# Performance work log

Hardware: AMD Instinct MI355X
Metric: run time of the kernel (lower is better)

Reference implementation:

```python
import jax, jax.numpy as jnp
import numpy as np

B, DIN, H1, H2 = 16384, 512, 256, 128
S, DC, DE, T, TE, GH = 4, 4, 2, 3, 2, 64
NDOM = DC * DE            # 8 domain experts total
ETOT = S + NDOM + TE      # 14 experts feeding each task gate


def setup_inputs() -> dict:
    key = jax.random.key(0)
    ks = jax.random.split(key, 20)
    w = lambda k, shape, fan: (jax.random.normal(k, shape, jnp.float32) / np.sqrt(fan).astype(np.float32))
    x = jax.random.normal(ks[0], (B, DIN), jnp.float32)
    domain_ids = jax.random.randint(ks[1], (B,), 0, DC, jnp.int64) if jax.config.jax_enable_x64 else jax.random.randint(ks[1], (B,), 0, DC, jnp.int32)
    return {
        "x": x,
        "domain_ids": domain_ids,
        # shared experts (stacked): input->256->128, ReLU on both layers
        "sW1": w(ks[2], (S, DIN, H1), DIN), "sb1": jnp.zeros((S, H1), jnp.float32),
        "sW2": w(ks[3], (S, H1, H2), H1),   "sb2": jnp.zeros((S, H2), jnp.float32),
        # domain experts, all domains stacked in order domain0..domainDC-1
        "dW1": w(ks[4], (NDOM, DIN, H1), DIN), "db1": jnp.zeros((NDOM, H1), jnp.float32),
        "dW2": w(ks[5], (NDOM, H1, H2), H1),   "db2": jnp.zeros((NDOM, H2), jnp.float32),
        # task experts, all tasks stacked task0..taskT-1
        "tW1": w(ks[6], (T * TE, DIN, H1), DIN), "tb1": jnp.zeros((T * TE, H1), jnp.float32),
        "tW2": w(ks[7], (T * TE, H1, H2), H1),   "tb2": jnp.zeros((T * TE, H2), jnp.float32),
        # task gates (stacked over tasks): input->64 (ReLU) -> ETOT (linear) -> softmax
        "gW1": w(ks[8], (T, DIN, GH), DIN), "gb1": jnp.zeros((T, GH), jnp.float32),
        "gW2": w(ks[9], (T, GH, ETOT), GH), "gb2": jnp.zeros((T, ETOT), jnp.float32),
    }


def _experts(x, W1, b1, W2, b2):
    # x: [B, DIN]; W1: [E, DIN, H1]; W2: [E, H1, H2] -> [B, E, H2]
    h = jax.nn.relu(jnp.einsum('bi,eih->beh', x, W1) + b1)
    return jax.nn.relu(jnp.einsum('beh,eho->beo', h, W2) + b2)


def reference(x, domain_ids, sW1, sb1, sW2, sb2, dW1, db1, dW2, db2,
              tW1, tb1, tW2, tb2, gW1, gb1, gW2, gb2):
    shared = _experts(x, sW1, sb1, sW2, sb2)          # [B, S, H2]
    domain = _experts(x, dW1, db1, dW2, db2)          # [B, NDOM, H2]
    task = _experts(x, tW1, tb1, tW2, tb2)            # [B, T*TE, H2]
    task = task.reshape(B, T, TE, H2)
    base = jnp.concatenate([shared, domain], axis=1)  # [B, S+NDOM, H2]
    base = jnp.broadcast_to(base[:, None], (B, T, S + NDOM, H2))
    all_experts = jnp.concatenate([base, task], axis=2)  # [B, T, ETOT, H2]
    # task gates
    gh = jax.nn.relu(jnp.einsum('bi,tig->btg', x, gW1) + gb1)
    gates = jax.nn.softmax(jnp.einsum('btg,tge->bte', gh, gW2) + gb2, axis=-1)  # [B, T, ETOT]
    out = jnp.einsum('bteh,bte->tbh', all_experts, gates)  # [T, B, H2]
    # note: the torch per-sample domain_weighted_output is computed then discarded;
    # only these task outputs are returned, and they do not depend on domain_ids.
    return tuple(out[t] for t in range(T))
```

## Files before the change

### kernel.cpp

```cpp
#include <hip/hip_runtime.h>
#include <hip/hip_bf16.h>

#define NB 16384
#define DIN 512
#define H1 256
#define H2 128
#define NE 18
#define NT 3
#define NGH 64
#define NETOT 14

typedef float f32x4 __attribute__((ext_vector_type(4)));
typedef short s16x8 __attribute__((ext_vector_type(8)));
typedef short s16x4 __attribute__((ext_vector_type(4)));
typedef unsigned short u16;
typedef unsigned int u32;

__device__ __forceinline__ u16 f2bf(float f) {
    union { float f; u32 u; } v; v.f = f;
    u32 r = v.u + 0x7fffu + ((v.u >> 16) & 1u);
    return (u16)(r >> 16);
}
__device__ __forceinline__ float bf2f(u16 u) {
    union { u32 u; float f; } v; v.u = ((u32)u) << 16;
    return v.f;
}
__device__ __forceinline__ u32 cvtpk(float a, float b) {
    u32 r;
    asm("v_cvt_pk_bf16_f32 %0, %1, %2" : "=v"(r) : "v"(a), "v"(b));
    return r;
}

#define GLDS16(g, l) __builtin_amdgcn_global_load_lds((const u32*)(g), (u32*)(l), 16, 0, 0)
#define VMCNT0_BARRIER() do { asm volatile("s_waitcnt vmcnt(0)" ::: "memory"); __builtin_amdgcn_s_barrier(); } while (0)

__global__ __launch_bounds__(256) void k_prep(
    const float* __restrict__ x, u16* __restrict__ xb,
    const float* __restrict__ sW1, const float* __restrict__ dW1, const float* __restrict__ tW1,
    const float* __restrict__ sW2, const float* __restrict__ dW2, const float* __restrict__ tW2,
    const float* __restrict__ gW1, u16* __restrict__ w1t, u16* __restrict__ w2t, u16* __restrict__ gw1t)
{
    __shared__ float lds[64 * 65];
    int bx = blockIdx.x;
    if (bx < 8192) {
        int i = (bx * 256 + threadIdx.x) * 4;
        float4 v = *reinterpret_cast<const float4*>(x + i);
        ushort4 o;
        o.x = f2bf(v.x); o.y = f2bf(v.y); o.z = f2bf(v.z); o.w = f2bf(v.w);
        *reinterpret_cast<ushort4*>(xb + i) = o;
        return;
    }
    int b = bx - 8192;
    const float* src; u16* dst; int K, N, k0, n0;
    if (b < 576) {
        int e = b >> 5, tile = b & 31;
        src = (e < 4) ? sW1 + (size_t)e * DIN * H1 : (e < 12) ? dW1 + (size_t)(e - 4) * DIN * H1
                                                              : tW1 + (size_t)(e - 12) * DIN * H1;
        dst = w1t + (size_t)e * H1 * DIN; K = DIN; N = H1;
        k0 = (tile >> 2) * 64; n0 = (tile & 3) * 64;
    } else if (b < 720) {
        int b2 = b - 576; int e = b2 >> 3, tile = b2 & 7;
        src = (e < 4) ? sW2 + (size_t)e * H1 * H2 : (e < 12) ? dW2 + (size_t)(e - 4) * H1 * H2
                                                             : tW2 + (size_t)(e - 12) * H1 * H2;
        dst = w2t + (size_t)e * H2 * H1; K = H1; N = H2;
        k0 = (tile >> 1) * 64; n0 = (tile & 1) * 64;
    } else {
        int b3 = b - 720; int t = b3 >> 3, tile = b3 & 7;
        src = gW1 + (size_t)t * DIN * NGH; dst = gw1t + (size_t)t * NGH * DIN; K = DIN; N = NGH;
        k0 = tile * 64; n0 = 0;
    }
    int t = threadIdx.x;
#pragma unroll
    for (int i = 0; i < 16; ++i) {
        int idx = i * 256 + t;
        int kk = idx >> 6, nn = idx & 63;
        lds[kk * 65 + nn] = src[(size_t)(k0 + kk) * N + n0 + nn];
    }
    __syncthreads();
#pragma unroll
    for (int i = 0; i < 16; ++i) {
        int idx = i * 256 + t;
        int nn = idx >> 6, kk = idx & 63;
        dst[(size_t)(n0 + nn) * K + k0 + kk] = f2bf(lds[kk * 65 + nn]);
    }
}

__global__ __launch_bounds__(512, 4) void k_expert(
    const u16* __restrict__ xb, const u16* __restrict__ w1t, const u16* __restrict__ w2t,
    const float* __restrict__ sb1, const float* __restrict__ db1, const float* __restrict__ tb1,
    const float* __restrict__ sb2, const float* __restrict__ db2, const float* __restrict__ tb2,
    u16* __restrict__ eout)
{
    __shared__ __align__(128) char smem[65536];

    const int bx = blockIdx.x;
    const int e  = bx >> 7;
    const int m0 = (bx & 127) * 128;
    const int tid = threadIdx.x;
    const int w = tid >> 6, lane = tid & 63;
    const int wm = w & 1, wn = w >> 1;
    const int l15 = lane & 15, q = lane >> 4;
    const int q16 = q * 16;
    const int swk = ((l15 >> 1) & 3) << 4;
    const int swh = (l15 & 7) << 4;

    const u16* xg  = xb + (size_t)m0 * DIN;
    const u16* w1g = w1t + (size_t)e * H1 * DIN;
    const u16* w2g = w2t + (size_t)e * H2 * H1;
    const float* b1p = (e < 4) ? sb1 + e * H1 : (e < 12) ? db1 + (e - 4) * H1 : tb1 + (e - 12) * H1;
    const float* b2p = (e < 4) ? sb2 + e * H2 : (e < 12) ? db2 + (e - 4) * H2 : tb2 + (e - 12) * H2;

    const int sr = lane >> 2, sc = lane & 3;
    const int soff = (sc ^ ((lane >> 3) & 3)) * 8;
    const u16* gx   = xg  + (size_t)(w * 16 + sr) * DIN + soff;
    const u16* gw1a = w1g + (size_t)(w * 32 + sr) * DIN + soff;
    const u16* gw1b = w1g + (size_t)(w * 32 + 16 + sr) * DIN + soff;
    const int lx  = w * 1024;
    const int lwa = w * 2048;
    const int lwb = w * 2048 + 1024;

    int offX[4], offW[4];
#pragma unroll
    for (int mi = 0; mi < 4; ++mi)
        offX[mi] = (wm * 64 + mi * 16 + l15) * 64 + (q16 ^ swk);
#pragma unroll
    for (int nj = 0; nj < 4; ++nj)
        offW[nj] = (wn * 64 + nj * 16 + l15) * 64 + (q16 ^ swk);

    f32x4 acc1[4][4];
#pragma unroll
    for (int i = 0; i < 4; ++i)
#pragma unroll
        for (int j = 0; j < 4; ++j) acc1[i][j] = (f32x4)0.f;

    GLDS16(gx, smem + lx);
    GLDS16(gw1a, smem + 16384 + lwa);
    GLDS16(gw1b, smem + 16384 + lwb);
    VMCNT0_BARRIER();
    for (int kt = 0; kt < 16; ++kt) {
        if (kt < 15) {
            const int nb = (kt + 1) & 1, ko = (kt + 1) * 32;
            GLDS16(gx + ko, smem + nb * 8192 + lx);
            GLDS16(gw1a + ko, smem + 16384 + nb * 16384 + lwa);
            GLDS16(gw1b + ko, smem + 16384 + nb * 16384 + lwb);
        }
        const char* xbase = smem + (kt & 1) * 8192;
        const char* wbase = smem + 16384 + (kt & 1) * 16384;
        s16x8 xf[4], wf[4];
#pragma unroll
        for (int mi = 0; mi < 4; ++mi) xf[mi] = *(const s16x8*)(xbase + offX[mi]);
#pragma unroll
        for (int nj = 0; nj < 4; ++nj) wf[nj] = *(const s16x8*)(wbase + offW[nj]);
        __builtin_amdgcn_s_setprio(1);
#pragma unroll
        for (int mi = 0; mi < 4; ++mi)
#pragma unroll
            for (int nj = 0; nj < 4; ++nj)
                acc1[mi][nj] = __builtin_amdgcn_mfma_f32_16x16x32_bf16(wf[nj], xf[mi], acc1[mi][nj], 0, 0, 0);
        __builtin_amdgcn_s_setprio(0);
        VMCNT0_BARRIER();
    }

#pragma unroll
    for (int mi = 0; mi < 4; ++mi) {
        const int m = wm * 64 + mi * 16 + l15;
        char* rowp = smem + m * 512;
#pragma unroll
        for (int nj = 0; nj < 4; ++nj) {
            const float4 bv = *reinterpret_cast<const float4*>(b1p + wn * 64 + nj * 16 + q * 4);
            float v0 = fmaxf(acc1[mi][nj][0] + bv.x, 0.f);
            float v1 = fmaxf(acc1[mi][nj][1] + bv.y, 0.f);
            float v2 = fmaxf(acc1[mi][nj][2] + bv.z, 0.f);
            float v3 = fmaxf(acc1[mi][nj][3] + bv.w, 0.f);
            uint2 hv; hv.x = cvtpk(v0, v1); hv.y = cvtpk(v2, v3);
            const int b = wn * 128 + nj * 32 + q * 8;
            *reinterpret_cast<uint2*>(rowp + (b ^ swh)) = hv;
        }
    }
    __syncthreads();

    f32x4 acc2[4][2];
#pragma unroll
    for (int i = 0; i < 4; ++i)
#pragma unroll
        for (int j = 0; j < 2; ++j) acc2[i][j] = (f32x4)0.f;
    const u16* w2p0 = w2g + (size_t)(wn * 32 + l15) * H1 + q * 8;
    const u16* w2p1 = w2g + (size_t)(wn * 32 + 16 + l15) * H1 + q * 8;
#pragma unroll
    for (int kt2 = 0; kt2 < 8; ++kt2) {
        s16x8 wf2[2], hf[4];
        wf2[0] = *(const s16x8*)(w2p0 + kt2 * 32);
        wf2[1] = *(const s16x8*)(w2p1 + kt2 * 32);
#pragma unroll
        for (int mi = 0; mi < 4; ++mi) {
            const int m = wm * 64 + mi * 16 + l15;
            hf[mi] = *(const s16x8*)(smem + m * 512 + ((kt2 * 64 + q16) ^ swh));
        }
#pragma unroll
        for (int mi = 0; mi < 4; ++mi)
#pragma unroll
            for (int pj = 0; pj < 2; ++pj)
                acc2[mi][pj] = __builtin_amdgcn_mfma_f32_16x16x32_bf16(hf[mi], wf2[pj], acc2[mi][pj], 0, 0, 0);
    }

    u16* eo = eout + ((size_t)e * NB + m0) * H2;
#pragma unroll
    for (int mi = 0; mi < 4; ++mi)
#pragma unroll
        for (int pj = 0; pj < 2; ++pj) {
            const int p = wn * 32 + pj * 16 + l15;
            const float bias = b2p[p];
#pragma unroll
            for (int r = 0; r < 4; ++r) {
                const int row = wm * 64 + mi * 16 + q * 4 + r;
                float v = acc2[mi][pj][r] + bias;
                eo[(size_t)row * H2 + p] = f2bf(v > 0.f ? v : 0.f);
            }
        }
}

__global__ __launch_bounds__(256) void k_gate(
    const u16* __restrict__ xb, const u16* __restrict__ gw1t,
    const float* __restrict__ gb1, const float* __restrict__ gw2, const float* __restrict__ gb2,
    float* __restrict__ gates)
{
    __shared__ __align__(16) char smem[51200];
    u16* xs  = reinterpret_cast<u16*>(smem);
    u16* g1s = reinterpret_cast<u16*>(smem) + 4608;
    float* ghs = reinterpret_cast<float*>(smem);

    int m0 = blockIdx.x * 64;
    int tid = threadIdx.x;
    int w = tid >> 6, lane = tid & 63;
    int wm = w & 1, wn = w >> 1;
    int l15 = lane & 15, lk = (lane >> 4) * 8, lr4 = (lane >> 4) * 4;

    f32x4 acc[2][6];
#pragma unroll
    for (int i = 0; i < 2; ++i)
#pragma unroll
        for (int j = 0; j < 6; ++j) acc[i][j] = (f32x4)0.f;

    const u16* xg = xb + (size_t)m0 * DIN;
    int srow = tid >> 3, su = (tid & 7) * 8;
    for (int kc = 0; kc < DIN / 64; ++kc) {
#pragma unroll
        for (int it = 0; it < 2; ++it) {
            int rr = srow + it * 32;
            *reinterpret_cast<uint4*>(&xs[rr * 72 + su]) =
                *reinterpret_cast<const uint4*>(xg + (size_t)rr * DIN + kc * 64 + su);
        }
#pragma unroll
        for (int it = 0; it < 6; ++it) {
            int rr = srow + it * 32;
            *reinterpret_cast<uint4*>(&g1s[rr * 72 + su]) =
                *reinterpret_cast<const uint4*>(gw1t + (size_t)rr * DIN + kc * 64 + su);
        }
        __syncthreads();
        s16x8 af[2][2], bfr[6][2];
#pragma unroll
        for (int mi = 0; mi < 2; ++mi)
#pragma unroll
            for (int kk = 0; kk < 2; ++kk)
                af[mi][kk] = *reinterpret_cast<const s16x8*>(&xs[(wm * 32 + mi * 16 + l15) * 72 + kk * 32 + lk]);
#pragma unroll
        for (int nj = 0; nj < 6; ++nj)
#pragma unroll
            for (int kk = 0; kk < 2; ++kk)
                bfr[nj][kk] = *reinterpret_cast<const s16x8*>(&g1s[(wn * 96 + nj * 16 + l15) * 72 + kk * 32 + lk]);
#pragma unroll
        for (int kk = 0; kk < 2; ++kk)
#pragma unroll
            for (int mi = 0; mi < 2; ++mi)
#pragma unroll
                for (int nj = 0; nj < 6; ++nj)
                    acc[mi][nj] = __builtin_amdgcn_mfma_f32_16x16x32_bf16(af[mi][kk], bfr[nj][kk], acc[mi][nj], 0, 0, 0);
        __syncthreads();
    }
#pragma unroll
    for (int mi = 0; mi < 2; ++mi)
#pragma unroll
        for (int nj = 0; nj < 6; ++nj) {
            int col = wn * 96 + nj * 16 + l15;
            float bias = gb1[col];
#pragma unroll
            for (int r = 0; r < 4; ++r) {
                int row = wm * 32 + mi * 16 + lr4 + r;
                float v = acc[mi][nj][r] + bias;
                ghs[row * 200 + col] = v > 0.f ? v : 0.f;
            }
        }
    __syncthreads();

    if (tid < 192) {
        int tt = tid >> 6, rr = tid & 63;
        float logit[NETOT];
#pragma unroll
        for (int e2 = 0; e2 < NETOT; ++e2) logit[e2] = gb2[tt * NETOT + e2];
        const float* g2 = gw2 + tt * NGH * NETOT;
        const float* gr = &ghs[rr * 200 + tt * 64];
        for (int g = 0; g < NGH; ++g) {
            float v = gr[g];
#pragma unroll
            for (int e2 = 0; e2 < NETOT; ++e2) logit[e2] += v * g2[g * NETOT + e2];
        }
        float m = logit[0];
#pragma unroll
        for (int e2 = 1; e2 < NETOT; ++e2) m = fmaxf(m, logit[e2]);
        float s = 0.f, p[NETOT];
#pragma unroll
        for (int e2 = 0; e2 < NETOT; ++e2) { p[e2] = __expf(logit[e2] - m); s += p[e2]; }
        float inv = 1.f / s;
        float* go = gates + (size_t)(m0 + rr) * (NT * NETOT) + tt * NETOT;
#pragma unroll
        for (int e2 = 0; e2 < NETOT; ++e2) go[e2] = p[e2] * inv;
    }
}

__global__ __launch_bounds__(256) void k_combine(
    const u16* __restrict__ eout, const float* __restrict__ gates, float* __restrict__ out)
{
    int tid = threadIdx.x;
    int lr = tid >> 5, hq = tid & 31;
    int b = blockIdx.x * 8 + lr;
    int h0 = hq * 4;
    const float* g = gates + (size_t)b * (NT * NETOT);
    float o0[4] = {0, 0, 0, 0}, o1[4] = {0, 0, 0, 0}, o2[4] = {0, 0, 0, 0};
#pragma unroll
    for (int e = 0; e < NE; ++e) {
        ushort4 ev = *reinterpret_cast<const ushort4*>(&eout[((size_t)e * NB + b) * H2 + h0]);
        float v0 = bf2f(ev.x), v1 = bf2f(ev.y), v2 = bf2f(ev.z), v3 = bf2f(ev.w);
        if (e < 12) {
            float wa = g[e], wb = g[NETOT + e], wc = g[2 * NETOT + e];
            o0[0] += wa * v0; o0[1] += wa * v1; o0[2] += wa * v2; o0[3] += wa * v3;
            o1[0] += wb * v0; o1[1] += wb * v1; o1[2] += wb * v2; o1[3] += wb * v3;
            o2[0] += wc * v0; o2[1] += wc * v1; o2[2] += wc * v2; o2[3] += wc * v3;
        } else {
            int t = (e - 12) >> 1, te = (e - 12) & 1;
            float wt = g[t * NETOT + 12 + te];
            float* ot = (t == 0) ? o0 : (t == 1) ? o1 : o2;
            ot[0] += wt * v0; ot[1] += wt * v1; ot[2] += wt * v2; ot[3] += wt * v3;
        }
    }
    size_t base = (size_t)b * H2 + h0;
    *reinterpret_cast<float4*>(&out[0 * (size_t)NB * H2 + base]) = make_float4(o0[0], o0[1], o0[2], o0[3]);
    *reinterpret_cast<float4*>(&out[1 * (size_t)NB * H2 + base]) = make_float4(o1[0], o1[1], o1[2], o1[3]);
    *reinterpret_cast<float4*>(&out[2 * (size_t)NB * H2 + base]) = make_float4(o2[0], o2[1], o2[2], o2[3]);
}

extern "C" void kernel_launch(void* const* d_in, const int* in_sizes, int n_in,
                              void* d_out, int out_size, void* d_ws, size_t ws_size,
                              hipStream_t stream)
{
    const float* x   = (const float*)d_in[0];
    const float* sW1 = (const float*)d_in[2];
    const float* sb1 = (const float*)d_in[3];
    const float* sW2 = (const float*)d_in[4];
    const float* sb2 = (const float*)d_in[5];
    const float* dW1 = (const float*)d_in[6];
    const float* db1 = (const float*)d_in[7];
    const float* dW2 = (const float*)d_in[8];
    const float* db2 = (const float*)d_in[9];
    const float* tW1 = (const float*)d_in[10];
    const float* tb1 = (const float*)d_in[11];
    const float* tW2 = (const float*)d_in[12];
    const float* tb2 = (const float*)d_in[13];
    const float* gW1 = (const float*)d_in[14];
    const float* gb1 = (const float*)d_in[15];
    const float* gW2 = (const float*)d_in[16];
    const float* gb2 = (const float*)d_in[17];

    char* ws = (char*)d_ws;
    u16*  xb    = (u16*)(ws + 0);
    u16*  w1t   = (u16*)(ws + 16777216);
    u16*  w2t   = (u16*)(ws + 21495808);
    u16*  gw1t  = (u16*)(ws + 22675456);
    float* gates = (float*)(ws + 22872064);
    u16*  eout  = (u16*)(ws + 25624576);

    k_prep<<<dim3(8936), dim3(256), 0, stream>>>(x, xb, sW1, dW1, tW1, sW2, dW2, tW2, gW1, w1t, w2t, gw1t);
    k_gate<<<dim3(NB / 64), dim3(256), 0, stream>>>(xb, gw1t, gb1, gW2, gb2, gates);
    k_expert<<<dim3(NE * (NB / 128)), dim3(512), 0, stream>>>(xb, w1t, w2t, sb1, db1, tb1, sb2, db2, tb2, eout);
    k_combine<<<dim3(NB / 8), dim3(256), 0, stream>>>(eout, gates, (float*)d_out);
}
```

Baseline: 183.2 us.

## Fuse gate kernel into expert kernel and retile experts to 256-thread blocks

Merges the gate network into the expert kernel as extra trailing blocks, removing one launch and letting gate work overlap expert GEMMs. The expert kernel moves from 512 threads with a 2x4 wave grid to 256 threads where each wave owns all 128 rows and a 64-column slice. It also loosens the pipeline to wait with vmcnt(6) so the next tile's loads stay in flight during compute. The hidden buffer drops the XOR swizzle for padded 528-byte rows. In exchange, per-thread accumulators double, raising register pressure, and occupancy falls to two blocks per CU.

After: 148.1 us. 1.24x faster.

```diff
diff --git a/kernel.cpp b/kernel.cpp
--- a/kernel.cpp
+++ b/kernel.cpp
@@ -12,7 +12,6 @@
 
 typedef float f32x4 __attribute__((ext_vector_type(4)));
 typedef short s16x8 __attribute__((ext_vector_type(8)));
-typedef short s16x4 __attribute__((ext_vector_type(4)));
 typedef unsigned short u16;
 typedef unsigned int u32;
 
@@ -32,7 +31,6 @@
 }
 
 #define GLDS16(g, l) __builtin_amdgcn_global_load_lds((const u32*)(g), (u32*)(l), 16, 0, 0)
-#define VMCNT0_BARRIER() do { asm volatile("s_waitcnt vmcnt(0)" ::: "memory"); __builtin_amdgcn_s_barrier(); } while (0)
 
 __global__ __launch_bounds__(256) void k_prep(
     const float* __restrict__ x, u16* __restrict__ xb,
@@ -85,24 +83,118 @@
     }
 }
 
-__global__ __launch_bounds__(512, 4) void k_expert(
+__global__ __launch_bounds__(256, 2) void k_expert_gate(
     const u16* __restrict__ xb, const u16* __restrict__ w1t, const u16* __restrict__ w2t,
     const float* __restrict__ sb1, const float* __restrict__ db1, const float* __restrict__ tb1,
     const float* __restrict__ sb2, const float* __restrict__ db2, const float* __restrict__ tb2,
-    u16* __restrict__ eout)
+    u16* __restrict__ eout,
+    const u16* __restrict__ gw1t, const float* __restrict__ gb1,
+    const float* __restrict__ gw2, const float* __restrict__ gb2, float* __restrict__ gates)
 {
-    __shared__ __align__(128) char smem[65536];
-
-    const int bx = blockIdx.x;
-    const int e  = bx >> 7;
-    const int m0 = (bx & 127) * 128;
+    __shared__ __align__(128) char smem[67584];
+
+    const int bid = blockIdx.x;
     const int tid = threadIdx.x;
+
+    if (bid >= 2304) {
+        u16* xs  = reinterpret_cast<u16*>(smem);
+        u16* g1s = reinterpret_cast<u16*>(smem) + 4608;
+        float* ghs = reinterpret_cast<float*>(smem);
+
+        int m0 = (bid - 2304) * 64;
+        int w = tid >> 6, lane = tid & 63;
+        int wm = w & 1, wn = w >> 1;
+        int l15 = lane & 15, lk = (lane >> 4) * 8, lr4 = (lane >> 4) * 4;
+
+        f32x4 acc[2][6];
+#pragma unroll
+        for (int i = 0; i < 2; ++i)
+#pragma unroll
+            for (int j = 0; j < 6; ++j) acc[i][j] = (f32x4)0.f;
+
+        const u16* xg = xb + (size_t)m0 * DIN;
+        int srow = tid >> 3, su = (tid & 7) * 8;
+        for (int kc = 0; kc < DIN / 64; ++kc) {
+#pragma unroll
+            for (int it = 0; it < 2; ++it) {
+                int rr = srow + it * 32;
+                *reinterpret_cast<uint4*>(&xs[rr * 72 + su]) =
+                    *reinterpret_cast<const uint4*>(xg + (size_t)rr * DIN + kc * 64 + su);
+            }
+#pragma unroll
+            for (int it = 0; it < 6; ++it) {
+                int rr = srow + it * 32;
+                *reinterpret_cast<uint4*>(&g1s[rr * 72 + su]) =
+                    *reinterpret_cast<const uint4*>(gw1t + (size_t)rr * DIN + kc * 64 + su);
+            }
+            __syncthreads();
+            s16x8 af[2][2], bfr[6][2];
+#pragma unroll
+            for (int mi = 0; mi < 2; ++mi)
+#pragma unroll
+                for (int kk = 0; kk < 2; ++kk)
+                    af[mi][kk] = *reinterpret_cast<const s16x8*>(&xs[(wm * 32 + mi * 16 + l15) * 72 + kk * 32 + lk]);
+#pragma unroll
+            for (int nj = 0; nj < 6; ++nj)
+#pragma unroll
+                for (int kk = 0; kk < 2; ++kk)
+                    bfr[nj][kk] = *reinterpret_cast<const s16x8*>(&g1s[(wn * 96 + nj * 16 + l15) * 72 + kk * 32 + lk]);
+#pragma unroll
+            for (int kk = 0; kk < 2; ++kk)
+#pragma unroll
+                for (int mi = 0; mi < 2; ++mi)
+#pragma unroll
+                    for (int nj = 0; nj < 6; ++nj)
+                        acc[mi][nj] = __builtin_amdgcn_mfma_f32_16x16x32_bf16(af[mi][kk], bfr[nj][kk], acc[mi][nj], 0, 0, 0);
+            __syncthreads();
+        }
+#pragma unroll
+        for (int mi = 0; mi < 2; ++mi)
+#pragma unroll
+            for (int nj = 0; nj < 6; ++nj) {
+                int col = wn * 96 + nj * 16 + l15;
+                float bias = gb1[col];
+#pragma unroll
+                for (int r = 0; r < 4; ++r) {
+                    int row = wm * 32 + mi * 16 + lr4 + r;
+                    float v = acc[mi][nj][r] + bias;
+                    ghs[row * 200 + col] = v > 0.f ? v : 0.f;
+                }
+            }
+        __syncthreads();
+
+        if (tid < 192) {
+            int tt = tid >> 6, rr = tid & 63;
+            float logit[NETOT];
+#pragma unroll
+            for (int e2 = 0; e2 < NETOT; ++e2) logit[e2] = gb2[tt * NETOT + e2];
+            const float* g2 = gw2 + tt * NGH * NETOT;
+            const float* gr = &ghs[rr * 200 + tt * 64];
+            for (int g = 0; g < NGH; ++g) {
+                float v = gr[g];
+#pragma unroll
+                for (int e2 = 0; e2 < NETOT; ++e2) logit[e2] += v * g2[g * NETOT + e2];
+            }
+            float m = logit[0];
+#pragma unroll
+            for (int e2 = 1; e2 < NETOT; ++e2) m = fmaxf(m, logit[e2]);
+            float s = 0.f, p[NETOT];
+#pragma unroll
+            for (int e2 = 0; e2 < NETOT; ++e2) { p[e2] = __expf(logit[e2] - m); s += p[e2]; }
+            float inv = 1.f / s;
+            float* go = gates + (size_t)(m0 + rr) * (NT * NETOT) + tt * NETOT;
+#pragma unroll
+            for (int e2 = 0; e2 < NETOT; ++e2) go[e2] = p[e2] * inv;
+        }
+        return;
+    }
+
+    const int e  = bid >> 7;
+    const int m0 = (bid & 127) * 128;
     const int w = tid >> 6, lane = tid & 63;
-    const int wm = w & 1, wn = w >> 1;
     const int l15 = lane & 15, q = lane >> 4;
     const int q16 = q * 16;
     const int swk = ((l15 >> 1) & 3) << 4;
-    const int swh = (l15 & 7) << 4;
 
     const u16* xg  = xb + (size_t)m0 * DIN;
     const u16* w1g = w1t + (size_t)e * H1 * DIN;
@@ -111,93 +203,105 @@
     const float* b2p = (e < 4) ? sb2 + e * H2 : (e < 12) ? db2 + (e - 4) * H2 : tb2 + (e - 12) * H2;
 
     const int sr = lane >> 2, sc = lane & 3;
-    const int soff = (sc ^ ((lane >> 3) & 3)) * 8;
-    const u16* gx   = xg  + (size_t)(w * 16 + sr) * DIN + soff;
-    const u16* gw1a = w1g + (size_t)(w * 32 + sr) * DIN + soff;
-    const u16* gw1b = w1g + (size_t)(w * 32 + 16 + sr) * DIN + soff;
-    const int lx  = w * 1024;
-    const int lwa = w * 2048;
-    const int lwb = w * 2048 + 1024;
-
-    int offX[4], offW[4];
-#pragma unroll
-    for (int mi = 0; mi < 4; ++mi)
-        offX[mi] = (wm * 64 + mi * 16 + l15) * 64 + (q16 ^ swk);
+    const u16* gx[2]; int lx[2];
+#pragma unroll
+    for (int j = 0; j < 2; ++j) {
+        int row = w * 32 + j * 16 + sr;
+        gx[j] = xg + (size_t)row * DIN + ((sc ^ ((row >> 1) & 3)) * 8);
+        lx[j] = w * 2048 + j * 1024;
+    }
+    const u16* gw1[4]; int lw1[4];
+#pragma unroll
+    for (int j = 0; j < 4; ++j) {
+        int row = w * 64 + j * 16 + sr;
+        gw1[j] = w1g + (size_t)row * DIN + ((sc ^ ((row >> 1) & 3)) * 8);
+        lw1[j] = 8192 + w * 4096 + j * 1024;
+    }
+
+    int offX[8], offW[4];
+#pragma unroll
+    for (int mi = 0; mi < 8; ++mi)
+        offX[mi] = (mi * 16 + l15) * 64 + (q16 ^ swk);
 #pragma unroll
     for (int nj = 0; nj < 4; ++nj)
-        offW[nj] = (wn * 64 + nj * 16 + l15) * 64 + (q16 ^ swk);
-
-    f32x4 acc1[4][4];
-#pragma unroll
-    for (int i = 0; i < 4; ++i)
+        offW[nj] = 8192 + (w * 64 + nj * 16 + l15) * 64 + (q16 ^ swk);
+
+    f32x4 acc1[8][4];
+#pragma unroll
+    for (int i = 0; i < 8; ++i)
 #pragma unroll
         for (int j = 0; j < 4; ++j) acc1[i][j] = (f32x4)0.f;
 
-    GLDS16(gx, smem + lx);
-    GLDS16(gw1a, smem + 16384 + lwa);
-    GLDS16(gw1b, smem + 16384 + lwb);
-    VMCNT0_BARRIER();
+#pragma unroll
+    for (int j = 0; j < 2; ++j) GLDS16(gx[j], smem + lx[j]);
+#pragma unroll
+    for (int j = 0; j < 4; ++j) GLDS16(gw1[j], smem + lw1[j]);
+
     for (int kt = 0; kt < 16; ++kt) {
         if (kt < 15) {
-            const int nb = (kt + 1) & 1, ko = (kt + 1) * 32;
-            GLDS16(gx + ko, smem + nb * 8192 + lx);
-            GLDS16(gw1a + ko, smem + 16384 + nb * 16384 + lwa);
-            GLDS16(gw1b + ko, smem + 16384 + nb * 16384 + lwb);
-        }
-        const char* xbase = smem + (kt & 1) * 8192;
-        const char* wbase = smem + 16384 + (kt & 1) * 16384;
-        s16x8 xf[4], wf[4];
-#pragma unroll
-        for (int mi = 0; mi < 4; ++mi) xf[mi] = *(const s16x8*)(xbase + offX[mi]);
-#pragma unroll
-        for (int nj = 0; nj < 4; ++nj) wf[nj] = *(const s16x8*)(wbase + offW[nj]);
+            const int nb = ((kt + 1) & 1) * 24576, ko = (kt + 1) * 32;
+#pragma unroll
+            for (int j = 0; j < 2; ++j) GLDS16(gx[j] + ko, smem + nb + lx[j]);
+#pragma unroll
+            for (int j = 0; j < 4; ++j) GLDS16(gw1[j] + ko, smem + nb + lw1[j]);
+            asm volatile("s_waitcnt vmcnt(6)" ::: "memory");
+        } else {
+            asm volatile("s_waitcnt vmcnt(0)" ::: "memory");
+        }
+        __builtin_amdgcn_s_barrier();
+
+        const char* cb = smem + (kt & 1) * 24576;
+        s16x8 xf[8], wf[4];
+#pragma unroll
+        for (int nj = 0; nj < 4; ++nj) wf[nj] = *(const s16x8*)(cb + offW[nj]);
+#pragma unroll
+        for (int mi = 0; mi < 8; ++mi) xf[mi] = *(const s16x8*)(cb + offX[mi]);
         __builtin_amdgcn_s_setprio(1);
 #pragma unroll
-        for (int mi = 0; mi < 4; ++mi)
+        for (int mi = 0; mi < 8; ++mi)
 #pragma unroll
             for (int nj = 0; nj < 4; ++nj)
                 acc1[mi][nj] = __builtin_amdgcn_mfma_f32_16x16x32_bf16(wf[nj], xf[mi], acc1[mi][nj], 0, 0, 0);
         __builtin_amdgcn_s_setprio(0);
-        VMCNT0_BARRIER();
-    }
-
-#pragma unroll
-    for (int mi = 0; mi < 4; ++mi) {
-        const int m = wm * 64 + mi * 16 + l15;
-        char* rowp = smem + m * 512;
+        asm volatile("s_waitcnt lgkmcnt(0)" ::: "memory");
+        __builtin_amdgcn_s_barrier();
+    }
+
+#pragma unroll
+    for (int mi = 0; mi < 8; ++mi) {
+        const int m = mi * 16 + l15;
+        char* rowp = smem + m * 528;
 #pragma unroll
         for (int nj = 0; nj < 4; ++nj) {
-            const float4 bv = *reinterpret_cast<const float4*>(b1p + wn * 64 + nj * 16 + q * 4);
+            const int n0 = w * 64 + nj * 16 + q * 4;
+            const float4 bv = *reinterpret_cast<const float4*>(b1p + n0);
             float v0 = fmaxf(acc1[mi][nj][0] + bv.x, 0.f);
             float v1 = fmaxf(acc1[mi][nj][1] + bv.y, 0.f);
             float v2 = fmaxf(acc1[mi][nj][2] + bv.z, 0.f);
             float v3 = fmaxf(acc1[mi][nj][3] + bv.w, 0.f);
             uint2 hv; hv.x = cvtpk(v0, v1); hv.y = cvtpk(v2, v3);
-            const int b = wn * 128 + nj * 32 + q * 8;
-            *reinterpret_cast<uint2*>(rowp + (b ^ swh)) = hv;
+            *reinterpret_cast<uint2*>(rowp + n0 * 2) = hv;
         }
     }
     __syncthreads();
 
-    f32x4 acc2[4][2];
-#pragma unroll
-    for (int i = 0; i < 4; ++i)
+    f32x4 acc2[8][2];
+#pragma unroll
+    for (int i = 0; i < 8; ++i)
 #pragma unroll
         for (int j = 0; j < 2; ++j) acc2[i][j] = (f32x4)0.f;
-    const u16* w2p0 = w2g + (size_t)(wn * 32 + l15) * H1 + q * 8;
-    const u16* w2p1 = w2g + (size_t)(wn * 32 + 16 + l15) * H1 + q * 8;
+    const u16* w2p0 = w2g + (size_t)(w * 32 + l15) * H1 + q * 8;
+    const u16* w2p1 = w2g + (size_t)(w * 32 + 16 + l15) * H1 + q * 8;
 #pragma unroll
     for (int kt2 = 0; kt2 < 8; ++kt2) {
-        s16x8 wf2[2], hf[4];
+        s16x8 wf2[2], hf[8];
         wf2[0] = *(const s16x8*)(w2p0 + kt2 * 32);
         wf2[1] = *(const s16x8*)(w2p1 + kt2 * 32);
 #pragma unroll
-        for (int mi = 0; mi < 4; ++mi) {
-            const int m = wm * 64 + mi * 16 + l15;
-            hf[mi] = *(const s16x8*)(smem + m * 512 + ((kt2 * 64 + q16) ^ swh));
-        }
-#pragma unroll
-        for (int mi = 0; mi < 4; ++mi)
+        for (int mi = 0; mi < 8; ++mi)
+            hf[mi] = *(const s16x8*)(smem + (mi * 16 + l15) * 528 + kt2 * 64 + q16);
+#pragma unroll
+        for (int mi = 0; mi < 8; ++mi)
 #pragma unroll
             for (int pj = 0; pj < 2; ++pj)
                 acc2[mi][pj] = __builtin_amdgcn_mfma_f32_16x16x32_bf16(hf[mi], wf2[pj], acc2[mi][pj], 0, 0, 0);
@@ -205,116 +309,18 @@
 
     u16* eo = eout + ((size_t)e * NB + m0) * H2;
 #pragma unroll
-    for (int mi = 0; mi < 4; ++mi)
+    for (int mi = 0; mi < 8; ++mi)
 #pragma unroll
         for (int pj = 0; pj < 2; ++pj) {
-            const int p = wn * 32 + pj * 16 + l15;
+            const int p = w * 32 + pj * 16 + l15;
             const float bias = b2p[p];
 #pragma unroll
             for (int r = 0; r < 4; ++r) {
-                const int row = wm * 64 + mi * 16 + q * 4 + r;
+                const int row = mi * 16 + q * 4 + r;
                 float v = acc2[mi][pj][r] + bias;
                 eo[(size_t)row * H2 + p] = f2bf(v > 0.f ? v : 0.f);
             }
         }
-}
-
-__global__ __launch_bounds__(256) void k_gate(
-    const u16* __restrict__ xb, const u16* __restrict__ gw1t,
-    const float* __restrict__ gb1, const float* __restrict__ gw2, const float* __restrict__ gb2,
-    float* __restrict__ gates)
-{
-    __shared__ __align__(16) char smem[51200];
-    u16* xs  = reinterpret_cast<u16*>(smem);
-    u16* g1s = reinterpret_cast<u16*>(smem) + 4608;
-    float* ghs = reinterpret_cast<float*>(smem);
-
-    int m0 = blockIdx.x * 64;
-    int tid = threadIdx.x;
-    int w = tid >> 6, lane = tid & 63;
-    int wm = w & 1, wn = w >> 1;
-    int l15 = lane & 15, lk = (lane >> 4) * 8, lr4 = (lane >> 4) * 4;
-
-    f32x4 acc[2][6];
-#pragma unroll
-    for (int i = 0; i < 2; ++i)
-#pragma unroll
-        for (int j = 0; j < 6; ++j) acc[i][j] = (f32x4)0.f;
-
-    const u16* xg = xb + (size_t)m0 * DIN;
-    int srow = tid >> 3, su = (tid & 7) * 8;
-    for (int kc = 0; kc < DIN / 64; ++kc) {
-#pragma unroll
-        for (int it = 0; it < 2; ++it) {
-            int rr = srow + it * 32;
-            *reinterpret_cast<uint4*>(&xs[rr * 72 + su]) =
-                *reinterpret_cast<const uint4*>(xg + (size_t)rr * DIN + kc * 64 + su);
-        }
-#pragma unroll
-        for (int it = 0; it < 6; ++it) {
-            int rr = srow + it * 32;
-            *reinterpret_cast<uint4*>(&g1s[rr * 72 + su]) =
-                *reinterpret_cast<const uint4*>(gw1t + (size_t)rr * DIN + kc * 64 + su);
-        }
-        __syncthreads();
-        s16x8 af[2][2], bfr[6][2];
-#pragma unroll
-        for (int mi = 0; mi < 2; ++mi)
-#pragma unroll
-            for (int kk = 0; kk < 2; ++kk)
-                af[mi][kk] = *reinterpret_cast<const s16x8*>(&xs[(wm * 32 + mi * 16 + l15) * 72 + kk * 32 + lk]);
-#pragma unroll
-        for (int nj = 0; nj < 6; ++nj)
-#pragma unroll
-            for (int kk = 0; kk < 2; ++kk)
-                bfr[nj][kk] = *reinterpret_cast<const s16x8*>(&g1s[(wn * 96 + nj * 16 + l15) * 72 + kk * 32 + lk]);
-#pragma unroll
-        for (int kk = 0; kk < 2; ++kk)
-#pragma unroll
-            for (int mi = 0; mi < 2; ++mi)
-#pragma unroll
-                for (int nj = 0; nj < 6; ++nj)
-                    acc[mi][nj] = __builtin_amdgcn_mfma_f32_16x16x32_bf16(af[mi][kk], bfr[nj][kk], acc[mi][nj], 0, 0, 0);
-        __syncthreads();
-    }
-#pragma unroll
-    for (int mi = 0; mi < 2; ++mi)
-#pragma unroll
-        for (int nj = 0; nj < 6; ++nj) {
-            int col = wn * 96 + nj * 16 + l15;
-            float bias = gb1[col];
-#pragma unroll
-            for (int r = 0; r < 4; ++r) {
-                int row = wm * 32 + mi * 16 + lr4 + r;
-                float v = acc[mi][nj][r] + bias;
-                ghs[row * 200 + col] = v > 0.f ? v : 0.f;
-            }
-        }
-    __syncthreads();
-
-    if (tid < 192) {
-        int tt = tid >> 6, rr = tid & 63;
-        float logit[NETOT];
-#pragma unroll
-        for (int e2 = 0; e2 < NETOT; ++e2) logit[e2] = gb2[tt * NETOT + e2];
-        const float* g2 = gw2 + tt * NGH * NETOT;
-        const float* gr = &ghs[rr * 200 + tt * 64];
-        for (int g = 0; g < NGH; ++g) {
-            float v = gr[g];
-#pragma unroll
-            for (int e2 = 0; e2 < NETOT; ++e2) logit[e2] += v * g2[g * NETOT + e2];
-        }
-        float m = logit[0];
-#pragma unroll
-        for (int e2 = 1; e2 < NETOT; ++e2) m = fmaxf(m, logit[e2]);
-        float s = 0.f, p[NETOT];
-#pragma unroll
-        for (int e2 = 0; e2 < NETOT; ++e2) { p[e2] = __expf(logit[e2] - m); s += p[e2]; }
-        float inv = 1.f / s;
-        float* go = gates + (size_t)(m0 + rr) * (NT * NETOT) + tt * NETOT;
-#pragma unroll
-        for (int e2 = 0; e2 < NETOT; ++e2) go[e2] = p[e2] * inv;
-    }
 }
 
 __global__ __launch_bounds__(256) void k_combine(
@@ -379,7 +385,7 @@
     u16*  eout  = (u16*)(ws + 25624576);
 
     k_prep<<<dim3(8936), dim3(256), 0, stream>>>(x, xb, sW1, dW1, tW1, sW2, dW2, tW2, gW1, w1t, w2t, gw1t);
-    k_gate<<<dim3(NB / 64), dim3(256), 0, stream>>>(xb, gw1t, gb1, gW2, gb2, gates);
-    k_expert<<<dim3(NE * (NB / 128)), dim3(512), 0, stream>>>(xb, w1t, w2t, sb1, db1, tb1, sb2, db2, tb2, eout);
+    k_expert_gate<<<dim3(2560), dim3(256), 0, stream>>>(xb, w1t, w2t, sb1, db1, tb1, sb2, db2, tb2,
+                                                        eout, gw1t, gb1, gW2, gb2, gates);
     k_combine<<<dim3(NB / 8), dim3(256), 0, stream>>>(eout, gates, (float*)d_out);
 }
```
